# Kernel tuning notes

Measured on AMD Instinct MI355X. Metric: run time of the kernel, lower is better.

## Reference

```python
import jax, jax.numpy as jnp
import numpy as np

NE, NU, E = 200000, 100000, 1000000
F_IN, H, OUT = 64, 128, 2
GRID_SIZE, K = 5, 3  # efficient-kan defaults: grid_size=5, spline_order=3
NB = GRID_SIZE + K    # number of b-spline bases per input feature = 8


def make_grid(in_features):
    h = 2.0 / GRID_SIZE  # grid_range [-1, 1]
    g = jnp.arange(-K, GRID_SIZE + K + 1, dtype=jnp.float32) * h - 1.0  # [GRID_SIZE+2K+1]
    return jnp.tile(g[None, :], (in_features, 1))  # [in, 12]


def b_splines(x, grid):
    # x: [N, in], grid: [in, G]; Cox-de Boor recursion -> [N, in, G-K-1]
    x = x[..., None]
    bases = ((x >= grid[:, :-1]) & (x < grid[:, 1:])).astype(x.dtype)
    for j in range(1, K + 1):
        bases = ((x - grid[:, :-(j + 1)]) / (grid[:, j:-1] - grid[:, :-(j + 1)])) * bases[..., :-1] \
              + ((grid[:, j + 1:] - x) / (grid[:, j + 1:] - grid[:, 1:-j])) * bases[..., 1:]
    return bases


def kan_linear(x, base_w, spline_w, scaler, grid):
    base = jax.nn.silu(x) @ base_w.T                       # [N, out]
    sw = spline_w * scaler[..., None]                      # [out, in, NB]
    spline = jnp.einsum('nik,oik->no', b_splines(x, grid), sw)
    return base + spline


def sage_conv(x_src, x_dst, ei, w_n, b_n, w_r):
    # PyG SAGEConv: lin_l(mean_j x_j) + lin_r(x_i); bias only on lin_l
    src, dst = ei[0], ei[1]
    msg = jnp.take(x_src, src, axis=0)                                  # [E, H] gather
    s = jax.ops.segment_sum(msg, dst, num_segments=x_dst.shape[0])      # scatter-sum
    cnt = jax.ops.segment_sum(jnp.ones(src.shape, x_src.dtype), dst, num_segments=x_dst.shape[0])
    mean = s / jnp.maximum(cnt, 1.0)[:, None]
    return mean @ w_n.T + b_n + x_dst @ w_r.T


def setup_inputs():
    key = jax.random.key(0)
    ks = jax.random.split(key, 40)
    inp = {}
    inp['x_email'] = jax.random.normal(ks[0], (NE, F_IN), jnp.float32)
    inp['ei_ue'] = jnp.stack([jax.random.randint(ks[1], (E,), 0, NU),
                              jax.random.randint(ks[2], (E,), 0, NE)])
    inp['ei_eu'] = jnp.stack([jax.random.randint(ks[3], (E,), 0, NE),
                              jax.random.randint(ks[4], (E,), 0, NU)])
    inp['w_email'] = jax.random.normal(ks[5], (H, F_IN), jnp.float32) * 0.05
    inp['b_email'] = jnp.zeros((H,), jnp.float32)
    inp['emb_user'] = jax.random.normal(ks[6], (NU, H), jnp.float32) * 0.05
    i = 7
    for name in ['l1_ue', 'l1_eu', 'l2_ue', 'l2_eu']:
        inp['w_' + name + '_n'] = jax.random.normal(ks[i], (H, H), jnp.float32) * 0.05; i += 1
        inp['b_' + name] = jnp.zeros((H,), jnp.float32)
        inp['w_' + name + '_r'] = jax.random.normal(ks[i], (H, H), jnp.float32) * 0.05; i += 1
    inp['kan1_base'] = jax.random.normal(ks[i], (64, H), jnp.float32) * 0.05; i += 1
    inp['kan1_spline'] = jax.random.normal(ks[i], (64, H, NB), jnp.float32) * 0.05; i += 1
    inp['kan1_scaler'] = 1.0 + jax.random.normal(ks[i], (64, H), jnp.float32) * 0.05; i += 1
    inp['grid1'] = make_grid(H)
    inp['kan2_base'] = jax.random.normal(ks[i], (OUT, 64), jnp.float32) * 0.05; i += 1
    inp['kan2_spline'] = jax.random.normal(ks[i], (OUT, 64, NB), jnp.float32) * 0.05; i += 1
    inp['kan2_scaler'] = 1.0 + jax.random.normal(ks[i], (OUT, 64), jnp.float32) * 0.05; i += 1
    inp['grid2'] = make_grid(64)
    return inp


def reference(x_email, ei_ue, ei_eu, w_email, b_email, emb_user,
              w_l1_ue_n, b_l1_ue, w_l1_ue_r, w_l1_eu_n, b_l1_eu, w_l1_eu_r,
              w_l2_ue_n, b_l2_ue, w_l2_ue_r, w_l2_eu_n, b_l2_eu, w_l2_eu_r,
              kan1_base, kan1_spline, kan1_scaler, grid1,
              kan2_base, kan2_spline, kan2_scaler, grid2):
    xe = x_email @ w_email.T + b_email      # email_lin
    xu = emb_user                            # embedding(arange(NU)) == full table
    # hetero SAGE layer 1 (to_hetero aggr='sum'; one inbound edge type per dst)
    e1 = jax.nn.relu(sage_conv(xu, xe, ei_ue, w_l1_ue_n, b_l1_ue, w_l1_ue_r))
    u1 = jax.nn.relu(sage_conv(xe, xu, ei_eu, w_l1_eu_n, b_l1_eu, w_l1_eu_r))
    # dropout(p=0.5) is identity in eval mode
    # layer 2: only the email output feeds the KAN head (user-dst conv2 output is unused)
    e2 = jax.nn.relu(sage_conv(u1, e1, ei_ue, w_l2_ue_n, b_l2_ue, w_l2_ue_r))
    h = kan_linear(e2, kan1_base, kan1_spline, kan1_scaler, grid1)
    out = kan_linear(h, kan2_base, kan2_spline, kan2_scaler, grid2)
    return out
```

## Files before the change

kernel.cpp:

```cpp
#include <hip/hip_runtime.h>
#include <hip/hip_bf16.h>

typedef __attribute__((ext_vector_type(8))) short short8;
typedef __attribute__((ext_vector_type(4))) float f32x4;

static constexpr int kNE  = 200000;
static constexpr int kNU  = 100000;
static constexpr int kE   = 1000000;
static constexpr int kGrpU = kNE / 8;
static constexpr int kGrpE = kNU / 8;

static constexpr long long SZ_NEH = (long long)kNE * 128;
static constexpr long long SZ_NUH = (long long)kNU * 128;
static constexpr long long O_B0   = 64;
static constexpr long long O_B1   = O_B0 + SZ_NEH;
static constexpr long long O_B2   = O_B1 + SZ_NEH;
static constexpr long long O_W    = O_B2 + SZ_NUH;
static constexpr long long O_BEM  = O_W;
static constexpr long long O_BL1  = O_BEM + 128;
static constexpr long long O_BEN  = O_BL1 + 128;
static constexpr long long O_BL2  = O_BEN + 128;
static constexpr long long O_GRID1= O_BL2 + 128;
static constexpr long long O_BASE2= O_GRID1 + 1536;
static constexpr long long O_GRID2= O_BASE2 + 128;
static constexpr long long O_SW2  = O_GRID2 + 768;
static constexpr long long I_CNT_UE = O_SW2 + 1024;
static constexpr long long I_CNT_EU = I_CNT_UE + kNE;
static constexpr long long I_RO_UE  = I_CNT_EU + kNU;
static constexpr long long I_RO_EU  = I_RO_UE + kNE;
static constexpr long long I_CUR_UE = I_RO_EU + kNU;
static constexpr long long I_CUR_EU = I_CUR_UE + kNE;
static constexpr long long I_SRT_UE = I_CUR_EU + kNU;
static constexpr long long I_SRT_EU = I_SRT_UE + kE;
static constexpr long long I_BSUM_UE= I_SRT_EU + kE;
static constexpr long long I_BOFF_UE= I_BSUM_UE + 256;
static constexpr long long I_BSUM_EU= I_BOFF_UE + 256;
static constexpr long long I_BOFF_EU= I_BSUM_EU + 256;
static constexpr long long FR_BASE_I= (I_BOFF_EU + 256 + 7) & ~7LL;
static constexpr long long U_WEM   = 0;
static constexpr long long U_W1N   = U_WEM + 8192;
static constexpr long long U_W1R   = U_W1N + 16384;
static constexpr long long U_WEN   = U_W1R + 16384;
static constexpr long long U_WER   = U_WEN + 16384;
static constexpr long long U_W2N   = U_WER + 16384;
static constexpr long long U_W2R   = U_W2N + 16384;
static constexpr long long U_BASE1 = U_W2R + 16384;
static constexpr long long U_SW1H  = U_BASE1 + 8192;
static constexpr long long U_SW1L  = U_SW1H + 65536;

__device__ __forceinline__ float bf2f(unsigned short u) {
    return __uint_as_float(((unsigned)u) << 16);
}
__device__ __forceinline__ unsigned short f2bf_rne(float f) {
    unsigned u = __float_as_uint(f);
    return (unsigned short)((u + 0x7fffu + ((u >> 16) & 1u)) >> 16);
}
__device__ __forceinline__ void split2(float x, unsigned short& hi, unsigned short& lo) {
    hi = f2bf_rne(x);
    lo = f2bf_rne(x - bf2f(hi));
}
__device__ __forceinline__ float btrunc(float x) {
    return __uint_as_float(__float_as_uint(x) & 0xffff0000u);
}
__device__ __forceinline__ unsigned pack_hi2(float x0, float x1) {
    return __builtin_amdgcn_perm(__float_as_uint(x1), __float_as_uint(x0), 0x07060302u);
}
__device__ __forceinline__ void split8_trunc(const float* __restrict__ xv, short8& ah, short8& al) {
    unsigned* hp = (unsigned*)&ah;
    unsigned* lp = (unsigned*)&al;
#pragma unroll
    for (int jp = 0; jp < 4; jp++) {
        const float x0 = xv[2 * jp], x1 = xv[2 * jp + 1];
        const float l0 = x0 - btrunc(x0), l1 = x1 - btrunc(x1);
        hp[jp] = pack_hi2(x0, x1);
        lp[jp] = pack_hi2(l0, l1);
    }
}
__device__ __forceinline__ int get_isbf(const unsigned* __restrict__ g) {
    return (g[0] == 0xC00CCCCDu) ? 0 : 1;
}

__device__ __forceinline__ void pack128_one(const void* __restrict__ src, unsigned short* __restrict__ dst,
                                            int K, int t, int isbf) {
    const int lane = t & 63;
    const int nt = (t >> 6) % 8;
    const int kt = (t >> 6) / 8;
    const int n = nt * 16 + (lane & 15);
    const int k0 = kt * 32 + (lane >> 4) * 8;
    unsigned short* d = dst + (((size_t)(kt * 8 + nt) * 64 + lane) << 3);
#pragma unroll
    for (int j = 0; j < 8; j++) {
        float f = isbf ? bf2f(((const unsigned short*)src)[(size_t)n * K + k0 + j])
                       : ((const float*)src)[(size_t)n * K + k0 + j];
        d[j] = f2bf_rne(f);
    }
}

__device__ __forceinline__ void base1_one(const void* __restrict__ src, unsigned short* __restrict__ dst,
                                          int t, int isbf) {
    const int lane = t & 63, nt = (t >> 6) & 3, kt = t >> 8;
    const int n = nt * 16 + (lane & 15);
    const int k0 = kt * 32 + (lane >> 4) * 8;
    unsigned short* d = dst + (((size_t)(kt * 4 + nt) * 64 + lane) << 3);
#pragma unroll
    for (int j = 0; j < 8; j++) {
        float f = isbf ? bf2f(((const unsigned short*)src)[n * 128 + k0 + j])
                       : ((const float*)src)[n * 128 + k0 + j];
        d[j] = f2bf_rne(f);
    }
}

__device__ __forceinline__ void sw1_one(const void* __restrict__ sp, const void* __restrict__ sc,
                                        unsigned short* __restrict__ dh, unsigned short* __restrict__ dl,
                                        int t, int isbf) {
    const int lane = t & 63, nt = (t >> 6) & 3, kt = t >> 8;
    const int n = nt * 16 + (lane & 15);
    const int k0 = kt * 32 + (lane >> 4) * 8;
    const float scal = isbf ? bf2f(((const unsigned short*)sc)[n * 128 + (k0 >> 3)])
                            : ((const float*)sc)[n * 128 + (k0 >> 3)];
    const size_t base = ((size_t)(kt * 4 + nt) * 64 + lane) << 3;
#pragma unroll
    for (int j = 0; j < 8; j++) {
        float f = isbf ? bf2f(((const unsigned short*)sp)[(size_t)n * 1024 + k0 + j])
                       : ((const float*)sp)[(size_t)n * 1024 + k0 + j];
        float p = f * scal;
        unsigned short hi, lo;
        split2(p, hi, lo);
        dh[base + j] = hi;
        dl[base + j] = lo;
    }
}

struct PrepArgs {
    const void* csrc[7];  int coff[7];  int cn[7];
    const void* psrc[7];  unsigned pdst[7];  int pK[7];
    const void* sp2;  const void* sc2;
    const void* b1src;  const void* swsp;  const void* swsc;
};

__global__ __launch_bounds__(256) void prep_kernel(PrepArgs A, float* __restrict__ wsf,
                                                   int* __restrict__ wsi,
                                                   unsigned short* __restrict__ fbase,
                                                   const unsigned* __restrict__ gdet) {
    const int isbf = get_isbf(gdet);
    const int t0 = blockIdx.x * 256 + threadIdx.x;
    const int gs = gridDim.x * 256;
    for (int i = t0; i < kNE + kNU; i += gs) wsi[I_CNT_UE + i] = 0;
    for (int t = 0; t < 7; t++) {
        const int n = A.cn[t];
        const void* s = A.csrc[t];
        float* d = wsf + A.coff[t];
        for (int i = t0; i < n; i += gs)
            d[i] = isbf ? bf2f(((const unsigned short*)s)[i]) : ((const float*)s)[i];
    }
    for (int i = t0; i < 1024; i += gs) {
        float a = isbf ? bf2f(((const unsigned short*)A.sp2)[i]) : ((const float*)A.sp2)[i];
        float b = isbf ? bf2f(((const unsigned short*)A.sc2)[i >> 3]) : ((const float*)A.sc2)[i >> 3];
        wsf[O_SW2 + i] = a * b;
    }
    for (int t = 0; t < 7; t++) {
        const int K = A.pK[t];
        const int tot = (K / 32) * 8 * 64;
        unsigned short* dst = fbase + A.pdst[t];
        const void* src = A.psrc[t];
        for (int i = t0; i < tot; i += gs) pack128_one(src, dst, K, i, isbf);
    }
    for (int i = t0; i < 1024; i += gs) base1_one(A.b1src, fbase + U_BASE1, i, isbf);
    for (int i = t0; i < 8192; i += gs)
        sw1_one(A.swsp, A.swsc, fbase + U_SW1H, fbase + U_SW1L, i, isbf);
}

__global__ __launch_bounds__(256) void hist_both(const int* __restrict__ ue, const int* __restrict__ eu,
                                                 int* __restrict__ cntU, int* __restrict__ cntE) {
    const int g = blockIdx.x & 7;
    const int loU = g * kGrpU, hiU = loU + kGrpU;
    const int loE = g * kGrpE, hiE = loE + kGrpE;
    const int stride = (gridDim.x >> 3) * 256;
    for (int i = (blockIdx.x >> 3) * 256 + threadIdx.x; i < kE; i += stride) {
        const int d = ue[kE + i];
        if (d >= loU && d < hiU) atomicAdd(&cntU[d], 1);
        const int d2 = eu[kE + i];
        if (d2 >= loE && d2 < hiE) atomicAdd(&cntE[d2], 1);
    }
}

__global__ __launch_bounds__(256) void scan1_both(const int* __restrict__ cntU, int* __restrict__ roU,
                                                  int* __restrict__ bsU, const int* __restrict__ cntE,
                                                  int* __restrict__ roE, int* __restrict__ bsE) {
    __shared__ int sc[256];
    int b = blockIdx.x;
    const int* cnt;  int* ro;  int* bsum;  int n;
    if (b < 196) { cnt = cntU; ro = roU; bsum = bsU; n = kNE; }
    else { b -= 196; cnt = cntE; ro = roE; bsum = bsE; n = kNU; }
    const int t = threadIdx.x;
    const int i0 = b * 1024 + t * 4;
    int c[4];
#pragma unroll
    for (int q = 0; q < 4; q++) c[q] = (i0 + q < n) ? cnt[i0 + q] : 0;
    int s = c[0] + c[1] + c[2] + c[3];
    sc[t] = s;
    __syncthreads();
    for (int off = 1; off < 256; off <<= 1) {
        int v = (t >= off) ? sc[t - off] : 0;
        __syncthreads();
        sc[t] += v;
        __syncthreads();
    }
    int run = sc[t] - s;
#pragma unroll
    for (int q = 0; q < 4; q++) {
        if (i0 + q < n) ro[i0 + q] = run;
        run += c[q];
    }
    if (t == 255) bsum[b] = sc[255];
}

__global__ __launch_bounds__(256) void scan2_both(const int* __restrict__ bsU, int* __restrict__ boU,
                                                  const int* __restrict__ bsE, int* __restrict__ boE) {
    __shared__ int sc[256];
    const int* bsum;  int* boff;  int nb;
    if (blockIdx.x == 0) { bsum = bsU; boff = boU; nb = 196; }
    else { bsum = bsE; boff = boE; nb = 98; }
    const int t = threadIdx.x;
    int s = (t < nb) ? bsum[t] : 0;
    sc[t] = s;
    __syncthreads();
    for (int off = 1; off < 256; off <<= 1) {
        int v = (t >= off) ? sc[t - off] : 0;
        __syncthreads();
        sc[t] += v;
        __syncthreads();
    }
    if (t < nb) boff[t] = sc[t] - s;
}

__global__ __launch_bounds__(256) void scan3_both(int* __restrict__ roU, int* __restrict__ curU,
                                                  const int* __restrict__ boU, int* __restrict__ roE,
                                                  int* __restrict__ curE, const int* __restrict__ boE) {
    const int stride = gridDim.x * blockDim.x;
    for (int i = blockIdx.x * blockDim.x + threadIdx.x; i < kNE + kNU; i += stride) {
        if (i < kNE) {
            int v = roU[i] + boU[i >> 10];
            roU[i] = v;
            curU[i] = v;
        } else {
            int j = i - kNE;
            int v = roE[j] + boE[j >> 10];
            roE[j] = v;
            curE[j] = v;
        }
    }
}

__global__ __launch_bounds__(256) void fill_both(const int* __restrict__ ue, const int* __restrict__ eu,
                                                 int* __restrict__ curU, int* __restrict__ srtU,
                                                 int* __restrict__ curE, int* __restrict__ srtE) {
    const int g = blockIdx.x & 7;
    const int loU = g * kGrpU, hiU = loU + kGrpU;
    const int loE = g * kGrpE, hiE = loE + kGrpE;
    const int stride = (gridDim.x >> 3) * 256;
    for (int i = (blockIdx.x >> 3) * 256 + threadIdx.x; i < kE; i += stride) {
        const int d = ue[kE + i];
        if (d >= loU && d < hiU) {
            const int pos = atomicAdd(&curU[d], 1);
            srtU[pos] = ue[i];
        }
        const int d2 = eu[kE + i];
        if (d2 >= loE && d2 < hiE) {
            const int pos = atomicAdd(&curE[d2], 1);
            srtE[pos] = eu[i];
        }
    }
}

template <int KD, bool RAW, int THREADS>
__device__ __forceinline__ void stage_tile(float (*Xs)[132], const void* __restrict__ Av, int r0, int N,
                                           int tid, int isbf) {
    constexpr int TPR = THREADS / 64;
    constexpr int per = KD / TPR;
    const int row = tid / TPR;
    const int cq = (tid % TPR) * per;
    const size_t gr = (size_t)min(r0 + row, N - 1);
    if (RAW && isbf) {
        const unsigned short* p = (const unsigned short*)Av + gr * KD + cq;
#pragma unroll
        for (int v = 0; v < per; v += 8) {
            short8 s = *(const short8*)(p + v);
#pragma unroll
            for (int j = 0; j < 8; j++) Xs[row][cq + v + j] = bf2f(((unsigned short*)&s)[j]);
        }
    } else {
        const float* p = (const float*)Av + gr * KD + cq;
#pragma unroll
        for (int v = 0; v < per; v += 4) *(float4*)&Xs[row][cq + v] = *(const float4*)(p + v);
    }
}

template <int KT, int NT>
__device__ __forceinline__ void gemm_phase(float (*Xs)[132], const unsigned short* __restrict__ Wf,
                                           f32x4* acc, int rowl, int q, int lane, int ntBase) {
#pragma unroll
    for (int kt = 0; kt < KT; kt++) {
        float xv[8];
        *(float4*)&xv[0] = *(const float4*)&Xs[rowl][kt * 32 + q * 8];
        *(float4*)&xv[4] = *(const float4*)&Xs[rowl][kt * 32 + q * 8 + 4];
        short8 ah, al;
        split8_trunc(xv, ah, al);
#pragma unroll
        for (int nt = 0; nt < NT; nt++) {
            short8 b = *(const short8*)(Wf + (((size_t)(kt * 8 + ntBase + nt) * 64 + lane) << 3));
            acc[nt] = __builtin_amdgcn_mfma_f32_16x16x32_bf16(ah, b, acc[nt], 0, 0, 0);
            acc[nt] = __builtin_amdgcn_mfma_f32_16x16x32_bf16(al, b, acc[nt], 0, 0, 0);
        }
    }
}

__global__ __launch_bounds__(256) void lin_xe(const void* __restrict__ A1,
                                              const unsigned short* __restrict__ W1f,
                                              const float* __restrict__ bias, float* __restrict__ out, int N,
                                              const unsigned* __restrict__ gdet) {
    __shared__ float Xs[64][132];
    const int tid = threadIdx.x;
    const int wave = tid >> 6, lane = tid & 63;
    const int m = lane & 15, q = lane >> 4;
    const int r0 = blockIdx.x * 64;
    const int isbf = get_isbf(gdet);
    const int rowl = wave * 16 + m;
    f32x4 acc[8] = {};

    stage_tile<64, true, 256>(Xs, A1, r0, N, tid, isbf);
    __syncthreads();
    gemm_phase<2, 8>(Xs, W1f, acc, rowl, q, lane, 0);

    float bv[8];
#pragma unroll
    for (int nt = 0; nt < 8; nt++) bv[nt] = bias[nt * 16 + m];
#pragma unroll
    for (int r = 0; r < 4; r++) {
        int grow = r0 + wave * 16 + q * 4 + r;
        if (grow < N) {
#pragma unroll
            for (int nt = 0; nt < 8; nt++)
                out[(size_t)grow * 128 + nt * 16 + m] = acc[nt][r] + bv[nt];
        }
    }
}

template <bool RAWG>
__device__ __forceinline__ float2 gload(const void* __restrict__ G, int s, int lane, int isbf) {
    if (RAWG && isbf) {
        const ushort2 v = *(const ushort2*)((const unsigned short*)G + (size_t)s * 128 + lane * 2);
        return make_float2(bf2f(v.x), bf2f(v.y));
    }
    return *(const float2*)((const float*)G + (size_t)s * 128 + lane * 2);
}

template <bool RAWG, bool RAW2>
__global__ __launch_bounds__(512, 8) void agglin_mfma(const void* __restrict__ Gsrc, const void* __restrict__ A2,
                                                   const unsigned short* __restrict__ W1f,
                                                   const unsigned short* __restrict__ W2f,
                                                   const float* __restrict__ bias, float* __restrict__ out,
                                                   const int* __restrict__ ro, const int* __restrict__ cnt,
                                                   const int* __restrict__ sorted, int N,
                                                   const unsigned* __restrict__ gdet) {
    __shared__ float Xs[64][132];
    const int tid = threadIdx.x;
    const int wave = tid >> 6, lane = tid & 63;
    const int m = lane & 15, q = lane >> 4;
    const int wg = wave >> 1;
    const int wh = wave & 1;
    const int r0 = blockIdx.x * 64;
    const int isbf = get_isbf(gdet);

    for (int rr = 0; rr < 8; rr++) {
        const int lrow = wave * 8 + rr;
        const int n = r0 + lrow;
        float ax = 0.f, ay = 0.f;
        if (n < N) {
            const int beg = ro[n];
            const int end = beg + cnt[n];
            float a1x = 0.f, a1y = 0.f, a2x = 0.f, a2y = 0.f, a3x = 0.f, a3y = 0.f;
            int p = beg;
            for (; p + 3 < end; p += 4) {
                const int s0 = sorted[p], s1 = sorted[p + 1], s2 = sorted[p + 2], s3 = sorted[p + 3];
                const float2 v0 = gload<RAWG>(Gsrc, s0, lane, isbf);
                const float2 v1 = gload<RAWG>(Gsrc, s1, lane, isbf);
                const float2 v2 = gload<RAWG>(Gsrc, s2, lane, isbf);
                const float2 v3 = gload<RAWG>(Gsrc, s3, lane, isbf);
                ax += v0.x;  ay += v0.y;
                a1x += v1.x; a1y += v1.y;
                a2x += v2.x; a2y += v2.y;
                a3x += v3.x; a3y += v3.y;
            }
            for (; p < end; p++) {
                const float2 v = gload<RAWG>(Gsrc, sorted[p], lane, isbf);
                ax += v.x;
                ay += v.y;
            }
            ax += a1x + a2x + a3x;
            ay += a1y + a2y + a3y;
            const int deg = end - beg;
            const float inv = (deg > 0) ? 1.f / (float)deg : 0.f;
            ax *= inv;
            ay *= inv;
        }
        Xs[lrow][lane * 2] = ax;
        Xs[lrow][lane * 2 + 1] = ay;
    }
    __syncthreads();

    const int rowl = wg * 16 + m;
    const int ntBase = wh * 4;
    f32x4 acc[4] = {};

    gemm_phase<4, 4>(Xs, W1f, acc, rowl, q, lane, ntBase);

    __syncthreads();
    stage_tile<128, RAW2, 512>(Xs, A2, r0, N, tid, isbf);
    __syncthreads();
    gemm_phase<4, 4>(Xs, W2f, acc, rowl, q, lane, ntBase);

    float bv[4];
#pragma unroll
    for (int nt = 0; nt < 4; nt++) bv[nt] = bias[(ntBase + nt) * 16 + m];
#pragma unroll
    for (int r = 0; r < 4; r++) {
        int grow = r0 + wg * 16 + q * 4 + r;
        if (grow < N) {
#pragma unroll
            for (int nt = 0; nt < 4; nt++) {
                float v = acc[nt][r] + bv[nt];
                out[(size_t)grow * 128 + (ntBase + nt) * 16 + m] = fmaxf(v, 0.f);
            }
        }
    }
}

__device__ __forceinline__ void bases8u(float x, float t0, float invh, float* __restrict__ b) {
    const float sp = (x - t0) * invh;
    const float fi = floorf(sp);
    const float u = sp - fi;
    const int i = (int)fi;
    const float u2 = u * u, u3 = u2 * u;
    const float v = 1.f - u;
    const float p0 = u3 * (1.f / 6.f);
    const float p1 = fmaf(-0.5f, u3, fmaf(0.5f, u2, fmaf(0.5f, u, 1.f / 6.f)));
    const float p2 = fmaf(0.5f, u3, fmaf(-1.f, u2, 2.f / 3.f));
    const float p3 = v * v * v * (1.f / 6.f);
#pragma unroll
    for (int j = 0; j < 8; j++) {
        float r = (i == j) ? p0 : 0.f;
        r = (i == j + 1) ? p1 : r;
        r = (i == j + 2) ? p2 : r;
        r = (i == j + 3) ? p3 : r;
        b[j] = r;
    }
}

__device__ __forceinline__ void bases8u_frag(float x, float t0, float invh, short8& bh, short8& bl) {
    const float sp = (x - t0) * invh;
    const float fi = floorf(sp);
    const float u = sp - fi;
    int i = (int)fi;
    i = max(-1, min(11, i));
    const float u2 = u * u, u3 = u2 * u;
    const float v = 1.f - u;
    const float p0 = u3 * (1.f / 6.f);
    const float p1 = fmaf(-0.5f, u3, fmaf(0.5f, u2, fmaf(0.5f, u, 1.f / 6.f)));
    const float p2 = fmaf(0.5f, u3, fmaf(-1.f, u2, 2.f / 3.f));
    const float p3 = v * (v * v) * (1.f / 6.f);
    const float q0 = p0 - btrunc(p0), q1 = p1 - btrunc(p1);
    const float q2 = p2 - btrunc(p2), q3 = p3 - btrunc(p3);
    const unsigned long long Ph = (((unsigned long long)pack_hi2(p1, p0)) << 32) | pack_hi2(p3, p2);
    const unsigned long long Pl = (((unsigned long long)pack_hi2(q1, q0)) << 32) | pack_hi2(q3, q2);
    const int t = 16 * i - 48;
    const unsigned sa = (unsigned)t & 63u;
    const unsigned sb = (unsigned)(-t) & 63u;
    const unsigned sc = (unsigned)(64 - t) & 63u;
    const unsigned sd = (unsigned)(t - 64) & 63u;
    const bool neg = t < 0;
    const bool ok0 = t >= -48;
    const bool lt64 = t < 64;
    const bool gt0 = t > 0;
    const bool lt128 = t < 128;
    const unsigned long long h0 = neg ? (ok0 ? (Ph >> sb) : 0ull) : (lt64 ? (Ph << sa) : 0ull);
    const unsigned long long h1 = neg ? 0ull : (lt64 ? (gt0 ? (Ph >> sc) : 0ull)
                                                     : (lt128 ? (Ph << sd) : 0ull));
    const unsigned long long g0 = neg ? (ok0 ? (Pl >> sb) : 0ull) : (lt64 ? (Pl << sa) : 0ull);
    const unsigned long long g1 = neg ? 0ull : (lt64 ? (gt0 ? (Pl >> sc) : 0ull)
                                                     : (lt128 ? (Pl << sd) : 0ull));
    unsigned long long* bhp = (unsigned long long*)&bh;
    unsigned long long* blp = (unsigned long long*)&bl;
    bhp[0] = h0; bhp[1] = h1;
    blp[0] = g0; blp[1] = g1;
}

__global__ __launch_bounds__(256) void kan1_mfma(const float* __restrict__ X,
                                                 const unsigned short* __restrict__ basef,
                                                 const unsigned short* __restrict__ swh,
                                                 const unsigned short* __restrict__ swl,
                                                 const float* __restrict__ grid, float* __restrict__ Hout) {
    __shared__ float Xs[64][128];
    const int tid = threadIdx.x;
    const int wave = tid >> 6, lane = tid & 63;
    const int m = lane & 15, q = lane >> 4;
    const int r0 = blockIdx.x * 64;

    const float t0 = grid[0];
    const float invh = 1.f / (grid[1] - grid[0]);

    {
        const int row = tid >> 2, cq = (tid & 3) * 32;
        const int sw = (row & 7) << 2;
        const float* p = &X[(size_t)(r0 + row) * 128 + cq];
#pragma unroll
        for (int v = 0; v < 8; v++) *(float4*)&Xs[row][(cq + v * 4) ^ sw] = *(const float4*)(p + v * 4);
    }
    __syncthreads();

    const int rowl = wave * 16 + m;
    const int swr = (rowl & 7) << 2;
    f32x4 acc[4] = {};

#pragma unroll
    for (int kt = 0; kt < 4; kt++) {
        float xv[8];
        *(float4*)&xv[0] = *(const float4*)&Xs[rowl][(kt * 32 + q * 8) ^ swr];
        *(float4*)&xv[4] = *(const float4*)&Xs[rowl][(kt * 32 + q * 8 + 4) ^ swr];
        float sv[8];
#pragma unroll
        for (int j = 0; j < 8; j++) {
            float x = xv[j];
            sv[j] = x / (1.f + __expf(-x));
        }
        short8 ah, al;
        split8_trunc(sv, ah, al);
#pragma unroll
        for (int nt = 0; nt < 4; nt++) {
            short8 b = *(const short8*)(basef + (((size_t)(kt * 4 + nt) * 64 + lane) << 3));
            acc[nt] = __builtin_amdgcn_mfma_f32_16x16x32_bf16(ah, b, acc[nt], 0, 0, 0);
            acc[nt] = __builtin_amdgcn_mfma_f32_16x16x32_bf16(al, b, acc[nt], 0, 0, 0);
        }
    }

    const unsigned short* __restrict__ whp = swh + ((size_t)lane << 3);
    const unsigned short* __restrict__ wlp = swl + ((size_t)lane << 3);
    short8 wAh[4], wAl[4], wBh[4], wBl[4];
#pragma unroll
    for (int nt = 0; nt < 4; nt++) {
        wAh[nt] = *(const short8*)(whp + nt * 512);
        wAl[nt] = *(const short8*)(wlp + nt * 512);
    }
    float xE = Xs[rowl][q ^ swr];
#pragma unroll 1
    for (int kt2 = 0; kt2 < 16; kt2++) {
        const int ko = 2 * kt2 + 1;
#pragma unroll
        for (int nt = 0; nt < 4; nt++) {
            wBh[nt] = *(const short8*)(whp + ko * 2048 + nt * 512);
            wBl[nt] = *(const short8*)(wlp + ko * 2048 + nt * 512);
        }
        const float xO = Xs[rowl][(ko * 4 + q) ^ swr];
        {
            short8 bh, bl;
            bases8u_frag(xE, t0, invh, bh, bl);
#pragma unroll
            for (int nt = 0; nt < 4; nt++) {
                acc[nt] = __builtin_amdgcn_mfma_f32_16x16x32_bf16(bh, wAh[nt], acc[nt], 0, 0, 0);
                acc[nt] = __builtin_amdgcn_mfma_f32_16x16x32_bf16(bl, wAh[nt], acc[nt], 0, 0, 0);
                acc[nt] = __builtin_amdgcn_mfma_f32_16x16x32_bf16(bh, wAl[nt], acc[nt], 0, 0, 0);
            }
        }
        if (kt2 < 15) {
            const int ke2 = 2 * kt2 + 2;
#pragma unroll
            for (int nt = 0; nt < 4; nt++) {
                wAh[nt] = *(const short8*)(whp + ke2 * 2048 + nt * 512);
                wAl[nt] = *(const short8*)(wlp + ke2 * 2048 + nt * 512);
            }
            xE = Xs[rowl][(ke2 * 4 + q) ^ swr];
        }
        {
            short8 bh, bl;
            bases8u_frag(xO, t0, invh, bh, bl);
#pragma unroll
            for (int nt = 0; nt < 4; nt++) {
                acc[nt] = __builtin_amdgcn_mfma_f32_16x16x32_bf16(bh, wBh[nt], acc[nt], 0, 0, 0);
                acc[nt] = __builtin_amdgcn_mfma_f32_16x16x32_bf16(bl, wBh[nt], acc[nt], 0, 0, 0);
                acc[nt] = __builtin_amdgcn_mfma_f32_16x16x32_bf16(bh, wBl[nt], acc[nt], 0, 0, 0);
            }
        }
    }

#pragma unroll
    for (int r = 0; r < 4; r++) {
        int grow = r0 + wave * 16 + q * 4 + r;
#pragma unroll
        for (int nt = 0; nt < 4; nt++) Hout[(size_t)grow * 64 + nt * 16 + m] = acc[nt][r];
    }
}

__global__ __launch_bounds__(256) void kan2_kernel(const float* __restrict__ h, const float* __restrict__ base2,
                                                   const float* __restrict__ sw2, const float* __restrict__ grid2,
                                                   void* __restrict__ out, const unsigned* __restrict__ gdet) {
    const int lane = threadIdx.x & 63;
    const int wid = (blockIdx.x * blockDim.x + threadIdx.x) >> 6;
    const int nw = (gridDim.x * blockDim.x) >> 6;
    const int k = lane;
    const float t0 = grid2[0];
    const float invh = 1.f / (grid2[1] - grid2[0]);
    const float wb0 = base2[k], wb1 = base2[64 + k];
    float ws0[8], ws1[8];
#pragma unroll
    for (int j = 0; j < 8; j++) { ws0[j] = sw2[k * 8 + j]; ws1[j] = sw2[512 + k * 8 + j]; }
    const int isbf = get_isbf(gdet);

    for (int n = wid; n < kNE; n += nw) {
        float x = h[(size_t)n * 64 + k];
        float sil = x / (1.f + __expf(-x));
        float b[8];
        bases8u(x, t0, invh, b);
        float o0 = sil * wb0, o1 = sil * wb1;
#pragma unroll
        for (int j = 0; j < 8; j++) {
            o0 = fmaf(b[j], ws0[j], o0);
            o1 = fmaf(b[j], ws1[j], o1);
        }
#pragma unroll
        for (int off = 32; off > 0; off >>= 1) {
            o0 += __shfl_down(o0, off, 64);
            o1 += __shfl_down(o1, off, 64);
        }
        if (lane == 0) {
            if (isbf) {
                __hip_bfloat16* ob = (__hip_bfloat16*)out;
                ob[(size_t)n * 2] = __float2bfloat16(o0);
                ob[(size_t)n * 2 + 1] = __float2bfloat16(o1);
            } else {
                ((float2*)out)[n] = make_float2(o0, o1);
            }
        }
    }
}

extern "C" void kernel_launch(void* const* d_in, const int* in_sizes, int n_in, void* d_out, int out_size,
                              void* d_ws, size_t ws_size, hipStream_t stream) {
    (void)in_sizes; (void)n_in; (void)out_size; (void)ws_size;
    float* wsf = (float*)d_ws;
    int* wsi = (int*)d_ws;
    unsigned short* fbase = (unsigned short*)(wsi + FR_BASE_I);
    const unsigned* gdet = (const unsigned*)d_in[21];

    PrepArgs A;
    const int csrc[7] = {4, 7, 10, 13, 21, 22, 25};
    const long long coff[7] = {O_BEM, O_BL1, O_BEN, O_BL2, O_GRID1, O_BASE2, O_GRID2};
    const int cn[7] = {128, 128, 128, 128, 1536, 128, 768};
    for (int t = 0; t < 7; t++) {
        A.csrc[t] = d_in[csrc[t]];
        A.coff[t] = (int)coff[t];
        A.cn[t] = cn[t];
    }
    const int psrc[7] = {3, 6, 8, 9, 11, 12, 14};
    const long long pdst[7] = {U_WEM, U_W1N, U_W1R, U_WEN, U_WER, U_W2N, U_W2R};
    const int pK[7] = {64, 128, 128, 128, 128, 128, 128};
    for (int t = 0; t < 7; t++) {
        A.psrc[t] = d_in[psrc[t]];
        A.pdst[t] = (unsigned)pdst[t];
        A.pK[t] = pK[t];
    }
    A.sp2 = d_in[23];
    A.sc2 = d_in[24];
    A.b1src = d_in[18];
    A.swsp = d_in[19];
    A.swsc = d_in[20];
    prep_kernel<<<512, 256, 0, stream>>>(A, wsf, wsi, fbase, gdet);

    const int* ei_ue = (const int*)d_in[1];
    const int* ei_eu = (const int*)d_in[2];

    hist_both<<<2048, 256, 0, stream>>>(ei_ue, ei_eu, wsi + I_CNT_UE, wsi + I_CNT_EU);
    scan1_both<<<294, 256, 0, stream>>>(wsi + I_CNT_UE, wsi + I_RO_UE, wsi + I_BSUM_UE,
                                        wsi + I_CNT_EU, wsi + I_RO_EU, wsi + I_BSUM_EU);
    scan2_both<<<2, 256, 0, stream>>>(wsi + I_BSUM_UE, wsi + I_BOFF_UE, wsi + I_BSUM_EU, wsi + I_BOFF_EU);
    scan3_both<<<512, 256, 0, stream>>>(wsi + I_RO_UE, wsi + I_CUR_UE, wsi + I_BOFF_UE,
                                        wsi + I_RO_EU, wsi + I_CUR_EU, wsi + I_BOFF_EU);
    fill_both<<<2048, 256, 0, stream>>>(ei_ue, ei_eu, wsi + I_CUR_UE, wsi + I_SRT_UE,
                                        wsi + I_CUR_EU, wsi + I_SRT_EU);

    lin_xe<<<3125, 256, 0, stream>>>(d_in[0], fbase + U_WEM, wsf + O_BEM, wsf + O_B0, kNE, gdet);

    agglin_mfma<true, false><<<3125, 512, 0, stream>>>(
        d_in[5], wsf + O_B0, fbase + U_W1N, fbase + U_W1R, wsf + O_BL1, wsf + O_B1,
        wsi + I_RO_UE, wsi + I_CNT_UE, wsi + I_SRT_UE, kNE, gdet);

    agglin_mfma<false, true><<<1563, 512, 0, stream>>>(
        wsf + O_B0, d_in[5], fbase + U_WEN, fbase + U_WER, wsf + O_BEN, wsf + O_B2,
        wsi + I_RO_EU, wsi + I_CNT_EU, wsi + I_SRT_EU, kNU, gdet);

    agglin_mfma<false, false><<<3125, 512, 0, stream>>>(
        wsf + O_B2, wsf + O_B1, fbase + U_W2N, fbase + U_W2R, wsf + O_BL2, wsf + O_B0,
        wsi + I_RO_UE, wsi + I_CNT_UE, wsi + I_SRT_UE, kNE, gdet);

    kan1_mfma<<<3125, 256, 0, stream>>>(wsf + O_B0, fbase + U_BASE1, fbase + U_SW1H, fbase + U_SW1L,
                                        wsf + O_GRID1, wsf + O_B1);
    kan2_kernel<<<2048, 256, 0, stream>>>(wsf + O_B1, wsf + O_BASE2, wsf + O_SW2, wsf + O_GRID2, d_out, gdet);
}
```

Measured before the change: 934.2 us.

## Interleave neighbor gathers across eight rows per wave in fused aggregation kernel

Each wave used to walk its 8 destination rows one after another, unrolling 4 neighbors per row. It now walks all 8 rows in lockstep, issuing one gather per row per iteration, so up to 8 independent memory loads are in flight. This hides gather latency even for low-degree rows. Scalar indices go through readfirstlane, and launch bounds drop from 8 to 6 waves per SIMD to leave room for the extra registers. The cost is wasted predicated loads for rows that finish early, since the loop runs until the highest-degree row is done, plus lower occupancy.

```diff
diff --git a/kernel.cpp b/kernel.cpp
--- a/kernel.cpp
+++ b/kernel.cpp
@@ -356,7 +356,7 @@
 }
 
 template <bool RAWG, bool RAW2>
-__global__ __launch_bounds__(512, 8) void agglin_mfma(const void* __restrict__ Gsrc, const void* __restrict__ A2,
+__global__ __launch_bounds__(512, 6) void agglin_mfma(const void* __restrict__ Gsrc, const void* __restrict__ A2,
                                                    const unsigned short* __restrict__ W1f,
                                                    const unsigned short* __restrict__ W2f,
                                                    const float* __restrict__ bias, float* __restrict__ out,
@@ -372,40 +372,48 @@
     const int r0 = blockIdx.x * 64;
     const int isbf = get_isbf(gdet);
 
-    for (int rr = 0; rr < 8; rr++) {
-        const int lrow = wave * 8 + rr;
-        const int n = r0 + lrow;
-        float ax = 0.f, ay = 0.f;
-        if (n < N) {
-            const int beg = ro[n];
-            const int end = beg + cnt[n];
-            float a1x = 0.f, a1y = 0.f, a2x = 0.f, a2y = 0.f, a3x = 0.f, a3y = 0.f;
-            int p = beg;
-            for (; p + 3 < end; p += 4) {
-                const int s0 = sorted[p], s1 = sorted[p + 1], s2 = sorted[p + 2], s3 = sorted[p + 3];
-                const float2 v0 = gload<RAWG>(Gsrc, s0, lane, isbf);
-                const float2 v1 = gload<RAWG>(Gsrc, s1, lane, isbf);
-                const float2 v2 = gload<RAWG>(Gsrc, s2, lane, isbf);
-                const float2 v3 = gload<RAWG>(Gsrc, s3, lane, isbf);
-                ax += v0.x;  ay += v0.y;
-                a1x += v1.x; a1y += v1.y;
-                a2x += v2.x; a2y += v2.y;
-                a3x += v3.x; a3y += v3.y;
+    {
+        int pos[8], end[8];
+        float ax[8], ay[8], inv[8];
+#pragma unroll
+        for (int r = 0; r < 8; r++) {
+            const int n = r0 + wave * 8 + r;
+            ax[r] = 0.f;
+            ay[r] = 0.f;
+            if (n < N) {
+                const int b = __builtin_amdgcn_readfirstlane(ro[n]);
+                const int c = __builtin_amdgcn_readfirstlane(cnt[n]);
+                pos[r] = b;
+                end[r] = b + c;
+                inv[r] = (c > 0) ? 1.f / (float)c : 0.f;
+            } else {
+                pos[r] = 0;
+                end[r] = 0;
+                inv[r] = 0.f;
             }
-            for (; p < end; p++) {
-                const float2 v = gload<RAWG>(Gsrc, sorted[p], lane, isbf);
-                ax += v.x;
-                ay += v.y;
+        }
+        bool any = true;
+        while (any) {
+            bool nxt = false;
+#pragma unroll
+            for (int r = 0; r < 8; r++) {
+                const bool act = pos[r] < end[r];
+                const int pidx = act ? pos[r] : max(end[r] - 1, 0);
+                const int s = __builtin_amdgcn_readfirstlane(sorted[pidx]);
+                const float2 v = gload<RAWG>(Gsrc, s, lane, isbf);
+                ax[r] += act ? v.x : 0.f;
+                ay[r] += act ? v.y : 0.f;
+                pos[r] += act ? 1 : 0;
+                nxt = nxt || act;
             }
-            ax += a1x + a2x + a3x;
-            ay += a1y + a2y + a3y;
-            const int deg = end - beg;
-            const float inv = (deg > 0) ? 1.f / (float)deg : 0.f;
-            ax *= inv;
-            ay *= inv;
-        }
-        Xs[lrow][lane * 2] = ax;
-        Xs[lrow][lane * 2 + 1] = ay;
+            any = nxt;
+        }
+#pragma unroll
+        for (int r = 0; r < 8; r++) {
+            const int lrow = wave * 8 + r;
+            Xs[lrow][lane * 2] = ax[r] * inv[r];
+            Xs[lrow][lane * 2 + 1] = ay[r] * inv[r];
+        }
     }
     __syncthreads();
 
```

New measurement: 1.038 ms. +11.1%, slower.
